# Optimization experiments

Measured on AMD Instinct MI355X. Metric: run time of the kernel, lower is better.

Reference implementation:

```python
import jax, jax.numpy as jnp
import numpy as np

B, T, D, H, S, Ms = 16, 512, 64, 128, 100, 20  # batch, time, input, controller, slots, slot width


def setup_inputs() -> dict:
    key = jax.random.key(0)
    ks = jax.random.split(key, 12)
    rn = lambda k, shape, s=0.08: (jax.random.normal(k, shape, dtype=jnp.float32) * s)
    inp = {}
    inp["inputs"] = jax.random.normal(ks[0], (B, T, D), dtype=jnp.float32)
    inp["memory"] = jax.random.normal(ks[1], (S, Ms), dtype=jnp.float32)
    # Keras LSTM params (gate order i, f, c, o)
    inp["lstm_kernel"] = rn(ks[2], (D, 4 * H))
    inp["lstm_rkernel"] = rn(ks[3], (H, 4 * H))
    inp["lstm_bias"] = jnp.zeros((4 * H,), jnp.float32)
    # 2 read heads: key Dense(H -> Ms)
    inp["read_Wk"] = rn(ks[4], (2, H, Ms)); inp["read_bk"] = jnp.zeros((2, Ms), jnp.float32)
    # 2 write heads: key / erase(sigmoid) / add Dense(H -> Ms)
    inp["write_Wk"] = rn(ks[5], (2, H, Ms)); inp["write_bk"] = jnp.zeros((2, Ms), jnp.float32)
    inp["write_We"] = rn(ks[6], (2, H, Ms)); inp["write_be"] = jnp.zeros((2, Ms), jnp.float32)
    inp["write_Wa"] = rn(ks[7], (2, H, Ms)); inp["write_ba"] = jnp.zeros((2, Ms), jnp.float32)
    return inp


def _lstm(x, Wk, Rk, b):
    # x: [B,T,D] -> h_seq: [B,T,H]; Keras gate order i,f,c,o
    xw = jnp.einsum('btd,dh->bth', x, Wk) + b  # precompute input projection
    h0 = jnp.zeros((x.shape[0], Rk.shape[0]), x.dtype)
    c0 = jnp.zeros_like(h0)

    def step(carry, xt):
        h, c = carry
        z = xt + h @ Rk  # [B,4H]
        i, f, g, o = jnp.split(z, 4, axis=-1)
        i = jax.nn.sigmoid(i); f = jax.nn.sigmoid(f)
        g = jnp.tanh(g); o = jax.nn.sigmoid(o)
        c = f * c + i * g
        h = o * jnp.tanh(c)
        return (h, c), h

    _, hs = jax.lax.scan(step, (h0, c0), jnp.swapaxes(xw, 0, 1))
    return jnp.swapaxes(hs, 0, 1)


def _l2n(x):
    # tf.nn.l2_normalize semantics with epsilon 1e-12
    return x / jnp.sqrt(jnp.maximum(jnp.sum(x * x, axis=-1, keepdims=True), 1e-12))


def _neg_cos(a, b):
    # tf.keras.losses.cosine_similarity returns NEGATIVE cosine
    return -jnp.sum(_l2n(a) * _l2n(b), axis=-1)


def reference(inputs, memory, lstm_kernel, lstm_rkernel, lstm_bias,
              read_Wk, read_bk, write_Wk, write_bk,
              write_We, write_be, write_Wa, write_ba):
    ctrl = _lstm(inputs, lstm_kernel, lstm_rkernel, lstm_bias)  # [B,T,H]

    # content-addressable reads (on pre-write memory, as in original)
    reads = []
    for i in range(2):
        k = jax.nn.softmax(jnp.einsum('bth,hm->btm', ctrl, read_Wk[i]) + read_bk[i], axis=-1)
        sim = _neg_cos(k[:, :, None, :], memory[None, None, :, :])  # [B,T,S]
        w = jax.nn.softmax(sim, axis=-1)
        reads.append(jnp.einsum('bts,sm->btm', w, memory))

    # content-addressable erase/add writes, applied per (batch, time) position
    mem = memory[None, None, :, :]  # broadcast to [B,T,S,Ms] lazily
    for i in range(2):
        k = jax.nn.softmax(jnp.einsum('bth,hm->btm', ctrl, write_Wk[i]) + write_bk[i], axis=-1)
        sim = _neg_cos(k[:, :, None, :], mem)  # [B,T,S]
        w = jax.nn.softmax(sim, axis=-1)
        e = jax.nn.sigmoid(jnp.einsum('bth,hm->btm', ctrl, write_We[i]) + write_be[i])
        a = jnp.einsum('bth,hm->btm', ctrl, write_Wa[i]) + write_ba[i]
        mem = (1.0 - w[..., None] * e[:, :, None, :]) * mem + w[..., None] * a[:, :, None, :]

    out = jnp.concatenate([ctrl] + reads, axis=-1)  # [B,T,H+2*Ms]
    return out, mem
```

## Files before the change

### kernel.cpp

```cpp
#include <hip/hip_runtime.h>
#include <hip/hip_bf16.h>

#define BB 16
#define TT 512
#define DD 64
#define HH 128
#define SS 100
#define MSZ 20
#define NROW (BB*TT)
#define FOURH 512

typedef __attribute__((ext_vector_type(8))) short bh8;
typedef __attribute__((ext_vector_type(4))) float fv4;

__device__ __forceinline__ float frcp(float x){ return __builtin_amdgcn_rcpf(x); }
__device__ __forceinline__ float sigmoidf_(float x){
    return frcp(1.0f + __expf(-x));
}
__device__ __forceinline__ float tanhf_(float x){
    float t = __expf(2.0f * x);
    return 1.0f - 2.0f * frcp(t + 1.0f);
}
__device__ __forceinline__ unsigned short f2bf(float f){
    __hip_bfloat16 h = __float2bfloat16(f);
    union { __hip_bfloat16 b; unsigned short u; } cv; cv.b = h;
    return cv.u;
}

__global__ __launch_bounds__(512) void k_xw(const float* __restrict__ inp,
        const float* __restrict__ Wk, const float* __restrict__ bias,
        float* __restrict__ xw){
    __shared__ float in_s[8 * DD];
    int tid = threadIdx.x;
    int r0 = blockIdx.x * 8;
    in_s[tid] = inp[(size_t)r0 * DD + tid];
    __syncthreads();
    int j = tid;
    float wreg[DD];
    #pragma unroll
    for (int d = 0; d < DD; ++d) wreg[d] = Wk[d * FOURH + j];
    float bv = bias[j];
    const float4* in4 = reinterpret_cast<const float4*>(in_s);
    #pragma unroll
    for (int r = 0; r < 8; ++r){
        float acc = bv;
        #pragma unroll
        for (int q = 0; q < DD/4; ++q){
            float4 iv = in4[r*(DD/4) + q];
            acc = fmaf(iv.x, wreg[4*q+0], acc);
            acc = fmaf(iv.y, wreg[4*q+1], acc);
            acc = fmaf(iv.z, wreg[4*q+2], acc);
            acc = fmaf(iv.w, wreg[4*q+3], acc);
        }
        xw[(size_t)(r0 + r) * FOURH + j] = acc;
    }
}

__global__ __launch_bounds__(512, 2) void k_scan(const float* __restrict__ xw,
        const float* __restrict__ Rk, float* __restrict__ ctrl){
    __shared__ __align__(16) unsigned short hb[2][2048];
    const int tid = threadIdx.x;
    const int b  = blockIdx.x;
    const int w  = tid >> 6;
    const int l  = tid & 63;
    const int q  = l >> 4;
    const int lo = l & 15;
    { uint4* z4 = (uint4*)&hb[0][0]; z4[tid] = make_uint4(0u,0u,0u,0u); }
    bh8 bf[4][4];
    #pragma unroll
    for (int Ti = 0; Ti < 4; ++Ti){
        const int col = Ti*128 + w*16 + lo;
        #pragma unroll
        for (int kk = 0; kk < 4; ++kk){
            union { unsigned short us[8]; bh8 v; } u;
            #pragma unroll
            for (int j = 0; j < 8; ++j)
                u.us[j] = f2bf(Rk[(size_t)(kk*32 + q*8 + j)*FOURH + col]);
            bf[Ti][kk] = u.v;
        }
    }
    const bool upd = (q == 0);
    const int  n   = w*16 + lo;
    const float* xb = xw + (size_t)b * TT * FOURH;
    float c0 = 0.0f;
    float xc0=0.f, xc1=0.f, xc2=0.f, xc3=0.f;
    if (upd){
        xc0 = xb[0*128 + n]; xc1 = xb[1*128 + n];
        xc2 = xb[2*128 + n]; xc3 = xb[3*128 + n];
    }
    const int swz = (lo & 7) << 4;
    __syncthreads();
    int p = 0;
    for (int t = 0; t < TT; ++t){
        const char* hbase = (const char*)&hb[0][0] + p*4096 + lo*256;
        union { uint4 u; bh8 v; } a0, a1, a2, a3;
        a0.u = *(const uint4*)(hbase + ((q*16 +   0) ^ swz));
        a1.u = *(const uint4*)(hbase + ((q*16 +  64) ^ swz));
        a2.u = *(const uint4*)(hbase + ((q*16 + 128) ^ swz));
        a3.u = *(const uint4*)(hbase + ((q*16 + 192) ^ swz));
        const int tn = (t+1 < TT) ? t+1 : t;
        float xn0=0.f, xn1=0.f, xn2=0.f, xn3=0.f;
        if (upd){
            const float* xr = xb + (size_t)tn * FOURH;
            xn0 = xr[0*128 + n]; xn1 = xr[1*128 + n];
            xn2 = xr[2*128 + n]; xn3 = xr[3*128 + n];
        }
        fv4 z0 = {0.f,0.f,0.f,0.f}, z1 = z0, z2 = z0, z3 = z0;
        z0 = __builtin_amdgcn_mfma_f32_16x16x32_bf16(a0.v, bf[0][0], z0, 0,0,0);
        z1 = __builtin_amdgcn_mfma_f32_16x16x32_bf16(a0.v, bf[1][0], z1, 0,0,0);
        z2 = __builtin_amdgcn_mfma_f32_16x16x32_bf16(a0.v, bf[2][0], z2, 0,0,0);
        z3 = __builtin_amdgcn_mfma_f32_16x16x32_bf16(a0.v, bf[3][0], z3, 0,0,0);
        z0 = __builtin_amdgcn_mfma_f32_16x16x32_bf16(a1.v, bf[0][1], z0, 0,0,0);
        z1 = __builtin_amdgcn_mfma_f32_16x16x32_bf16(a1.v, bf[1][1], z1, 0,0,0);
        z2 = __builtin_amdgcn_mfma_f32_16x16x32_bf16(a1.v, bf[2][1], z2, 0,0,0);
        z3 = __builtin_amdgcn_mfma_f32_16x16x32_bf16(a1.v, bf[3][1], z3, 0,0,0);
        z0 = __builtin_amdgcn_mfma_f32_16x16x32_bf16(a2.v, bf[0][2], z0, 0,0,0);
        z1 = __builtin_amdgcn_mfma_f32_16x16x32_bf16(a2.v, bf[1][2], z1, 0,0,0);
        z2 = __builtin_amdgcn_mfma_f32_16x16x32_bf16(a2.v, bf[2][2], z2, 0,0,0);
        z3 = __builtin_amdgcn_mfma_f32_16x16x32_bf16(a2.v, bf[3][2], z3, 0,0,0);
        z0 = __builtin_amdgcn_mfma_f32_16x16x32_bf16(a3.v, bf[0][3], z0, 0,0,0);
        z1 = __builtin_amdgcn_mfma_f32_16x16x32_bf16(a3.v, bf[1][3], z1, 0,0,0);
        z2 = __builtin_amdgcn_mfma_f32_16x16x32_bf16(a3.v, bf[2][3], z2, 0,0,0);
        z3 = __builtin_amdgcn_mfma_f32_16x16x32_bf16(a3.v, bf[3][3], z3, 0,0,0);
        if (upd){
            float zi = z0[0] + xc0;
            float zf = z1[0] + xc1;
            float zg = z2[0] + xc2;
            float zo = z3[0] + xc3;
            float ig = sigmoidf_(zi);
            float fg = sigmoidf_(zf);
            float gg = tanhf_   (zg);
            float og = sigmoidf_(zo);
            c0 = fg * c0 + ig * gg;
            float h = og * tanhf_(c0);
            ctrl[((size_t)b*TT + t)*HH + n] = h;
            *(unsigned short*)((char*)&hb[0][0] + (p^1)*4096 + 2*n) = f2bf(h);
            xc0 = xn0; xc1 = xn1; xc2 = xn2; xc3 = xn3;
        }
        p ^= 1;
        __syncthreads();
    }
}

__global__ __launch_bounds__(320) void k_proj(const float* __restrict__ ctrl,
        const float* __restrict__ rWk, const float* __restrict__ rbk,
        const float* __restrict__ wWk, const float* __restrict__ wbk,
        const float* __restrict__ wWe, const float* __restrict__ wbe,
        const float* __restrict__ wWa, const float* __restrict__ wba,
        float* __restrict__ proj, float* __restrict__ out){
    __shared__ float cs[16 * HH];
    int tid = threadIdx.x;
    int r0 = blockIdx.x * 16;
    for (int idx = tid; idx < 16 * HH; idx += 320){
        float v = ctrl[(size_t)r0 * HH + idx];
        cs[idx] = v;
        int r = idx >> 7, k = idx & 127;
        out[(size_t)(r0 + r) * 168 + k] = v;
    }
    __syncthreads();
    int j = tid % 160;
    int rh = tid / 160;
    int p = j / MSZ, m = j % MSZ;
    const float* Wp; const float* bp;
    switch (p){
        case 0:  Wp = rWk;            bp = rbk;        break;
        case 1:  Wp = rWk + HH*MSZ;   bp = rbk + MSZ;  break;
        case 2:  Wp = wWk;            bp = wbk;        break;
        case 3:  Wp = wWk + HH*MSZ;   bp = wbk + MSZ;  break;
        case 4:  Wp = wWe;            bp = wbe;        break;
        case 5:  Wp = wWe + HH*MSZ;   bp = wbe + MSZ;  break;
        case 6:  Wp = wWa;            bp = wba;        break;
        default: Wp = wWa + HH*MSZ;   bp = wba + MSZ;  break;
    }
    float wv[HH];
    #pragma unroll
    for (int k = 0; k < HH; ++k) wv[k] = Wp[k * MSZ + m];
    float bv = bp[m];
    #pragma unroll
    for (int r = 0; r < 8; ++r){
        int row = rh * 8 + r;
        float acc = bv;
        const float4* c4 = reinterpret_cast<const float4*>(cs + row * HH);
        #pragma unroll
        for (int q = 0; q < HH/4; ++q){
            float4 cv = c4[q];
            acc = fmaf(cv.x, wv[4*q+0], acc);
            acc = fmaf(cv.y, wv[4*q+1], acc);
            acc = fmaf(cv.z, wv[4*q+2], acc);
            acc = fmaf(cv.w, wv[4*q+3], acc);
        }
        proj[(size_t)(r0 + row) * 160 + j] = acc;
    }
}

__device__ __forceinline__ float blocksum128(float v, float* red){
    #pragma unroll
    for (int o = 1; o < 64; o <<= 1) v += __shfl_xor(v, o, 64);
    int tid = threadIdx.x;
    if ((tid & 63) == 0) red[tid >> 6] = v;
    __syncthreads();
    float s = red[0] + red[1];
    __syncthreads();
    return s;
}

__global__ __launch_bounds__(128) void k_heads(const float* __restrict__ proj,
        const float* __restrict__ memory, float* __restrict__ out,
        float* __restrict__ outmem){
    __shared__ float mem0[SS * MSZ];
    __shared__ float rn[SS];
    __shared__ float khat[4][MSZ];
    __shared__ float ea[4][MSZ];
    __shared__ float wrd[2][SS];
    __shared__ float red[2];
    __shared__ float pz[160];
    int tid = threadIdx.x;
    int bt = blockIdx.x;
    for (int idx = tid; idx < SS * MSZ; idx += 128) mem0[idx] = memory[idx];
    for (int idx = tid; idx < 160; idx += 128) pz[idx] = proj[(size_t)bt * 160 + idx];
    __syncthreads();
    if (tid < SS){
        float s2 = 0.0f;
        #pragma unroll
        for (int m = 0; m < MSZ; ++m){ float v = mem0[tid*MSZ + m]; s2 = fmaf(v, v, s2); }
        rn[tid] = rsqrtf(fmaxf(s2, 1e-12f));
    }
    {
        int g = tid >> 5, lm = tid & 31;
        float z = (lm < MSZ) ? pz[g*MSZ + lm] : 0.0f;
        float e = (lm < MSZ) ? __expf(z) : 0.0f;
        float ssum = e;
        #pragma unroll
        for (int o = 1; o < 32; o <<= 1) ssum += __shfl_xor(ssum, o, 32);
        float kv = e / ssum;
        float qs = kv * kv;
        #pragma unroll
        for (int o = 1; o < 32; o <<= 1) qs += __shfl_xor(qs, o, 32);
        float kn = kv * rsqrtf(fmaxf(qs, 1e-12f));
        if (lm < MSZ) khat[g][lm] = kn;
        float z2 = (lm < MSZ) ? pz[80 + g*MSZ + lm] : 0.0f;
        float v2 = (g < 2) ? sigmoidf_(z2) : z2;
        if (lm < MSZ) ea[g][lm] = v2;
    }
    __syncthreads();
    bool act = tid < SS;
    int s = tid;
    float d0 = 0.f, d1 = 0.f, dw = 0.f;
    if (act){
        #pragma unroll
        for (int m = 0; m < MSZ; ++m){
            float mv = mem0[s*MSZ + m];
            d0 = fmaf(khat[0][m], mv, d0);
            d1 = fmaf(khat[1][m], mv, d1);
            dw = fmaf(khat[2][m], mv, dw);
        }
    }
    float rns = act ? rn[s] : 0.0f;
    float e0 = act ? __expf(-rns * d0) : 0.0f;
    float e1 = act ? __expf(-rns * d1) : 0.0f;
    float ew = act ? __expf(-rns * dw) : 0.0f;
    float sum0 = blocksum128(e0, red);
    float sum1 = blocksum128(e1, red);
    float sumw = blocksum128(ew, red);
    if (act){ wrd[0][s] = e0 / sum0; wrd[1][s] = e1 / sum1; }
    float w0 = ew / sumw;
    float m1[MSZ];
    float n1 = 0.f, dkw = 0.f;
    if (act){
        #pragma unroll
        for (int m = 0; m < MSZ; ++m){
            float mv = mem0[s*MSZ + m];
            float v = fmaf(-w0 * ea[0][m], mv, mv);
            v = fmaf(w0, ea[2][m], v);
            m1[m] = v;
            n1 = fmaf(v, v, n1);
            dkw = fmaf(khat[3][m], v, dkw);
        }
    }
    float rn1 = rsqrtf(fmaxf(n1, 1e-12f));
    float e1w = act ? __expf(-rn1 * dkw) : 0.0f;
    float sum1w = blocksum128(e1w, red);
    float w1 = e1w / sum1w;
    if (act){
        float buf[MSZ];
        #pragma unroll
        for (int m = 0; m < MSZ; ++m){
            float v = m1[m];
            float v2 = fmaf(-w1 * ea[1][m], v, v);
            v2 = fmaf(w1, ea[3][m], v2);
            buf[m] = v2;
        }
        float4* dst = reinterpret_cast<float4*>(outmem + ((size_t)bt * SS + s) * MSZ);
        #pragma unroll
        for (int q = 0; q < MSZ/4; ++q)
            dst[q] = make_float4(buf[4*q], buf[4*q+1], buf[4*q+2], buf[4*q+3]);
    }
    __syncthreads();
    if (tid < 2 * MSZ){
        int hd = tid / MSZ, m = tid % MSZ;
        float acc = 0.0f;
        for (int s2 = 0; s2 < SS; ++s2)
            acc = fmaf(wrd[hd][s2], mem0[s2*MSZ + m], acc);
        out[(size_t)bt * 168 + 128 + hd*MSZ + m] = acc;
    }
}

extern "C" void kernel_launch(void* const* d_in, const int* in_sizes, int n_in,
                              void* d_out, int out_size, void* d_ws, size_t ws_size,
                              hipStream_t stream){
    const float* inputs = (const float*)d_in[0];
    const float* memory = (const float*)d_in[1];
    const float* Wk     = (const float*)d_in[2];
    const float* Rk     = (const float*)d_in[3];
    const float* bias   = (const float*)d_in[4];
    const float* rWk    = (const float*)d_in[5];
    const float* rbk    = (const float*)d_in[6];
    const float* wWk    = (const float*)d_in[7];
    const float* wbk    = (const float*)d_in[8];
    const float* wWe    = (const float*)d_in[9];
    const float* wbe    = (const float*)d_in[10];
    const float* wWa    = (const float*)d_in[11];
    const float* wba    = (const float*)d_in[12];

    float* out    = (float*)d_out;
    float* outmem = out + (size_t)NROW * 168;
    float* xw   = outmem;
    float* ctrl = (float*)d_ws;
    float* proj = ctrl + (size_t)NROW * HH;

    k_xw  <<<NROW/8,  512, 0, stream>>>(inputs, Wk, bias, xw);
    k_scan<<<BB,      512, 0, stream>>>(xw, Rk, ctrl);
    k_proj<<<NROW/16, 320, 0, stream>>>(ctrl, rWk, rbk, wWk, wbk, wWe, wbe, wWa, wba, proj, out);
    k_heads<<<NROW,   128, 0, stream>>>(proj, memory, out, outmem);
}
```

Before: 330.4 us.

## Interleave gate projections and shrink LSTM hidden-state buffer to single row

The input-projection kernel now writes the four gate values for each hidden unit contiguously, so the scan loads them with a single float4 per step instead of four scalar loads. The hidden-state LDS buffer shrinks from a 16-row padded, swizzled tile to one row. Only lane 0 of each A-row group loads h, and the other rows are fed zeros. The xw term is folded into the MFMA accumulator's initial value instead of being added afterwards. The intent is to cut per-step LDS traffic and global load count on the serial recurrence; any other consumer of xw now depends on the new interleaved layout.

```diff
diff --git a/kernel.cpp b/kernel.cpp
--- a/kernel.cpp
+++ b/kernel.cpp
@@ -36,6 +36,7 @@
     in_s[tid] = inp[(size_t)r0 * DD + tid];
     __syncthreads();
     int j = tid;
+    int n = j & 127, g = j >> 7;
     float wreg[DD];
     #pragma unroll
     for (int d = 0; d < DD; ++d) wreg[d] = Wk[d * FOURH + j];
@@ -52,20 +53,20 @@
             acc = fmaf(iv.z, wreg[4*q+2], acc);
             acc = fmaf(iv.w, wreg[4*q+3], acc);
         }
-        xw[(size_t)(r0 + r) * FOURH + j] = acc;
+        xw[(size_t)(r0 + r) * FOURH + n*4 + g] = acc;
     }
 }
 
 __global__ __launch_bounds__(512, 2) void k_scan(const float* __restrict__ xw,
         const float* __restrict__ Rk, float* __restrict__ ctrl){
-    __shared__ __align__(16) unsigned short hb[2][2048];
+    __shared__ __align__(16) unsigned short hb[2][HH];
     const int tid = threadIdx.x;
     const int b  = blockIdx.x;
     const int w  = tid >> 6;
     const int l  = tid & 63;
     const int q  = l >> 4;
     const int lo = l & 15;
-    { uint4* z4 = (uint4*)&hb[0][0]; z4[tid] = make_uint4(0u,0u,0u,0u); }
+    if (tid < 2*HH) hb[tid >> 7][tid & 127] = 0;
     bh8 bf[4][4];
     #pragma unroll
     for (int Ti = 0; Ti < 4; ++Ti){
@@ -80,32 +81,30 @@
         }
     }
     const bool upd = (q == 0);
+    const bool rdh = (lo == 0);
     const int  n   = w*16 + lo;
-    const float* xb = xw + (size_t)b * TT * FOURH;
+    const float4* xb4 = reinterpret_cast<const float4*>(xw) + (size_t)b*TT*HH + n;
     float c0 = 0.0f;
-    float xc0=0.f, xc1=0.f, xc2=0.f, xc3=0.f;
-    if (upd){
-        xc0 = xb[0*128 + n]; xc1 = xb[1*128 + n];
-        xc2 = xb[2*128 + n]; xc3 = xb[3*128 + n];
-    }
-    const int swz = (lo & 7) << 4;
+    float4 xc = upd ? xb4[0] : make_float4(0.f,0.f,0.f,0.f);
     __syncthreads();
     int p = 0;
     for (int t = 0; t < TT; ++t){
-        const char* hbase = (const char*)&hb[0][0] + p*4096 + lo*256;
         union { uint4 u; bh8 v; } a0, a1, a2, a3;
-        a0.u = *(const uint4*)(hbase + ((q*16 +   0) ^ swz));
-        a1.u = *(const uint4*)(hbase + ((q*16 +  64) ^ swz));
-        a2.u = *(const uint4*)(hbase + ((q*16 + 128) ^ swz));
-        a3.u = *(const uint4*)(hbase + ((q*16 + 192) ^ swz));
+        a0.u = make_uint4(0u,0u,0u,0u);
+        a1.u = a0.u; a2.u = a0.u; a3.u = a0.u;
+        if (rdh){
+            const uint4* hr = reinterpret_cast<const uint4*>(&hb[p][0]);
+            a0.u = hr[q];
+            a1.u = hr[q + 4];
+            a2.u = hr[q + 8];
+            a3.u = hr[q + 12];
+        }
         const int tn = (t+1 < TT) ? t+1 : t;
-        float xn0=0.f, xn1=0.f, xn2=0.f, xn3=0.f;
-        if (upd){
-            const float* xr = xb + (size_t)tn * FOURH;
-            xn0 = xr[0*128 + n]; xn1 = xr[1*128 + n];
-            xn2 = xr[2*128 + n]; xn3 = xr[3*128 + n];
-        }
-        fv4 z0 = {0.f,0.f,0.f,0.f}, z1 = z0, z2 = z0, z3 = z0;
+        float4 xn = upd ? xb4[(size_t)tn * HH] : make_float4(0.f,0.f,0.f,0.f);
+        fv4 z0 = {upd ? xc.x : 0.f, 0.f, 0.f, 0.f};
+        fv4 z1 = {upd ? xc.y : 0.f, 0.f, 0.f, 0.f};
+        fv4 z2 = {upd ? xc.z : 0.f, 0.f, 0.f, 0.f};
+        fv4 z3 = {upd ? xc.w : 0.f, 0.f, 0.f, 0.f};
         z0 = __builtin_amdgcn_mfma_f32_16x16x32_bf16(a0.v, bf[0][0], z0, 0,0,0);
         z1 = __builtin_amdgcn_mfma_f32_16x16x32_bf16(a0.v, bf[1][0], z1, 0,0,0);
         z2 = __builtin_amdgcn_mfma_f32_16x16x32_bf16(a0.v, bf[2][0], z2, 0,0,0);
@@ -123,19 +122,15 @@
         z2 = __builtin_amdgcn_mfma_f32_16x16x32_bf16(a3.v, bf[2][3], z2, 0,0,0);
         z3 = __builtin_amdgcn_mfma_f32_16x16x32_bf16(a3.v, bf[3][3], z3, 0,0,0);
         if (upd){
-            float zi = z0[0] + xc0;
-            float zf = z1[0] + xc1;
-            float zg = z2[0] + xc2;
-            float zo = z3[0] + xc3;
-            float ig = sigmoidf_(zi);
-            float fg = sigmoidf_(zf);
-            float gg = tanhf_   (zg);
-            float og = sigmoidf_(zo);
+            float ig = sigmoidf_(z0[0]);
+            float fg = sigmoidf_(z1[0]);
+            float gg = tanhf_   (z2[0]);
+            float og = sigmoidf_(z3[0]);
             c0 = fg * c0 + ig * gg;
             float h = og * tanhf_(c0);
             ctrl[((size_t)b*TT + t)*HH + n] = h;
-            *(unsigned short*)((char*)&hb[0][0] + (p^1)*4096 + 2*n) = f2bf(h);
-            xc0 = xn0; xc1 = xn1; xc2 = xn2; xc3 = xn3;
+            hb[p ^ 1][n] = f2bf(h);
+            xc = xn;
         }
         p ^= 1;
         __syncthreads();
```

New measurement: 356.3 us. 1.08x slower.
